# Optimization experiments

Hardware: AMD Instinct MI355X
Metric: run time of the kernel (lower is better)

## Reference

```python
import math
import jax, jax.numpy as jnp
import numpy as np

N0 = N1 = 100000
E = 200000
IN = OUT = 128
H = 8
DK = OUT // H
T = 2
R = 3


def setup_inputs() -> dict:
    key = jax.random.key(0)
    ks = jax.random.split(key, 24)
    s = 1.0 / math.sqrt(IN)
    inp = {
        'h0': jax.random.normal(ks[0], (N0, IN), jnp.float32),
        'h1': jax.random.normal(ks[1], (N1, IN), jnp.float32),
        'kw': jax.random.normal(ks[2], (T, IN, OUT), jnp.float32) * s,
        'kb': jax.random.normal(ks[3], (T, OUT), jnp.float32) * 0.01,
        'qw': jax.random.normal(ks[4], (T, IN, OUT), jnp.float32) * s,
        'qb': jax.random.normal(ks[5], (T, OUT), jnp.float32) * 0.01,
        'vw': jax.random.normal(ks[6], (T, IN, OUT), jnp.float32) * s,
        'vb': jax.random.normal(ks[7], (T, OUT), jnp.float32) * 0.01,
        'aw': jax.random.normal(ks[8], (T, OUT, OUT), jnp.float32) * (1.0 / math.sqrt(OUT)),
        'ab': jax.random.normal(ks[9], (T, OUT), jnp.float32) * 0.01,
        'rel_att': jax.random.normal(ks[10], (R, H, DK, DK), jnp.float32) * (1.0 / math.sqrt(DK)),
        'rel_msg': jax.random.normal(ks[11], (R, H, DK, DK), jnp.float32) * (1.0 / math.sqrt(DK)),
        'rel_pri': jnp.ones((R, H), jnp.float32),
        'skip': jnp.ones((T,), jnp.float32),
        'src0': jax.random.randint(ks[12], (E,), 0, N1, jnp.int32),  # author -> paper
        'dst0': jax.random.randint(ks[13], (E,), 0, N0, jnp.int32),
        'src1': jax.random.randint(ks[14], (E,), 0, N0, jnp.int32),  # paper -> author
        'dst1': jax.random.randint(ks[15], (E,), 0, N1, jnp.int32),
        'src2': jax.random.randint(ks[16], (E,), 0, N0, jnp.int32),  # paper -> paper
        'dst2': jax.random.randint(ks[17], (E,), 0, N0, jnp.int32),
    }
    return inp


def _edge_softmax(score, dst, n_dst):
    # segment softmax normalized by destination node (norm_by='dst')
    m = jax.ops.segment_max(score, dst, num_segments=n_dst)
    e = jnp.exp(score - m[dst])
    s = jax.ops.segment_sum(e, dst, num_segments=n_dst)
    return e / s[dst]


def reference(h0, h1, kw, kb, qw, qb, vw, vb, aw, ab, rel_att, rel_msg,
              rel_pri, skip, src0, dst0, src1, dst1, src2, dst2):
    n_heads, d_k = rel_att.shape[1], rel_att.shape[2]
    sqrt_dk = math.sqrt(d_k)
    hs = (h0, h1)
    Ns = (h0.shape[0], h1.shape[0])
    # per-type K/Q/V projections, reshaped to [N, H, d_k]
    k = [(hs[t] @ kw[t] + kb[t]).reshape(-1, n_heads, d_k) for t in range(2)]
    q = [(hs[t] @ qw[t] + qb[t]).reshape(-1, n_heads, d_k) for t in range(2)]
    v = [(hs[t] @ vw[t] + vb[t]).reshape(-1, n_heads, d_k) for t in range(2)]
    # (relation id, src node type, dst node type, src idx, dst idx)
    rels = ((0, 1, 0, src0, dst0), (1, 0, 1, src1, dst1), (2, 0, 0, src2, dst2))
    agg = {0: [], 1: []}
    for r, st, dt, s_idx, d_idx in rels:
        kk = jnp.einsum('nij,ijk->nik', k[st], rel_att[r])
        vv = jnp.einsum('nij,ijk->nik', v[st], rel_msg[r])
        score = (q[dt][d_idx] * kk[s_idx]).sum(-1) * rel_pri[r] / sqrt_dk  # [E,H]
        attn = _edge_softmax(score, d_idx, Ns[dt])
        msg = vv[s_idx] * attn[..., None]  # [E,H,d_k]
        agg[dt].append(jax.ops.segment_sum(msg, d_idx, num_segments=Ns[dt]))
    outs = []
    for t in range(2):
        tt = sum(agg[t]) / len(agg[t])  # cross_reducer='mean'
        tt = tt.reshape(Ns[t], n_heads * d_k)
        trans = tt @ aw[t] + ab[t]  # dropout in eval mode -> identity
        alpha = jax.nn.sigmoid(skip[t])
        outs.append(trans * alpha + hs[t] * (1.0 - alpha))
    return jnp.stack(outs)  # [2, N, out_dim] (N0 == N1)
```

## Files before the change

### kernel.cpp

```cpp
#include <hip/hip_runtime.h>
#include <stdint.h>

typedef __attribute__((ext_vector_type(8))) short s16x8;
typedef __attribute__((ext_vector_type(4))) float f32x4;

__device__ __forceinline__ ushort f2bf(float x) {
  union { float f; uint32_t u; } v; v.f = x;
  uint32_t r = v.u + 0x7FFFu + ((v.u >> 16) & 1u);
  return (ushort)(r >> 16);
}
__device__ __forceinline__ float bf2f(ushort u) {
  union { uint32_t u; float f; } v; v.u = ((uint32_t)u) << 16; return v.f;
}

__device__ __forceinline__ void barrier_lds_only() {
  asm volatile("s_waitcnt lgkmcnt(0)" ::: "memory");
  __builtin_amdgcn_s_barrier();
}

__global__ __launch_bounds__(256) void prep_weights(
    const float* __restrict__ kw, const float* __restrict__ kb,
    const float* __restrict__ qw, const float* __restrict__ qb,
    const float* __restrict__ vw, const float* __restrict__ vb,
    const float* __restrict__ aw, const float* __restrict__ ab,
    const float* __restrict__ rel_att, const float* __restrict__ rel_msg,
    ushort* __restrict__ WT, float* __restrict__ BIAS)
{
  int slot = blockIdx.x, tid = threadIdx.x;
  const float* W; const float* b; const float* rel = nullptr;
  switch (slot) {
    case 0: W = qw;         b = qb;       break;
    case 1: W = qw + 16384; b = qb + 128; break;
    case 2: W = kw + 16384; b = kb + 128; rel = rel_att + 0*2048; break;
    case 3: W = kw;         b = kb;       rel = rel_att + 1*2048; break;
    case 4: W = kw;         b = kb;       rel = rel_att + 2*2048; break;
    case 5: W = vw + 16384; b = vb + 128; rel = rel_msg + 0*2048; break;
    case 6: W = vw;         b = vb;       rel = rel_msg + 1*2048; break;
    case 7: W = vw;         b = vb;       rel = rel_msg + 2*2048; break;
    case 8: W = aw;         b = ab;       break;
    default: W = aw + 16384; b = ab + 128; break;
  }
  ushort* out = WT + slot * 16384;
  for (int e = tid; e < 16384; e += 256) {
    int c = e >> 7, k = e & 127;
    float val;
    if (!rel) {
      val = W[k*128 + c];
    } else {
      int h = c >> 4, cc = c & 15;
      float s = 0.f;
      #pragma unroll
      for (int j = 0; j < 16; j++) s += W[k*128 + h*16 + j] * rel[h*256 + j*16 + cc];
      val = s;
    }
    out[c*128 + k] = f2bf(val);
  }
  if (tid < 128) {
    int c = tid; float val;
    if (!rel) {
      val = b[c];
    } else {
      int h = c >> 4, cc = c & 15;
      float s = 0.f;
      #pragma unroll
      for (int j = 0; j < 16; j++) s += b[h*16 + j] * rel[h*256 + j*16 + cc];
      val = s;
    }
    BIAS[slot*128 + c] = val;
  }
}

__global__ __launch_bounds__(256) void proj_fused(
    const float* __restrict__ h0, const float* __restrict__ h1,
    const ushort* __restrict__ WT, const float* __restrict__ BIAS,
    ushort* __restrict__ P, int N)
{
  __shared__ ushort ALDS0[64 * 132];
  __shared__ ushort ALDS1[64 * 132];

  int src_t = blockIdx.y;
  const float* A = src_t ? h1 : h0;
  int nslots = src_t ? 3 : 5;
  unsigned smap = src_t ? 0x521u : 0x76430u;

  int tid = threadIdx.x;
  int lane = tid & 63;
  int wave = tid >> 6;
  int lr = lane & 15, lh = lane >> 4;
  int colbase = (wave & 1) * 64;
  int rowhalf = wave >> 1;

  int base = blockIdx.x * 64;
  if (base >= N) return;

  s16x8 af[2][4];
  #pragma unroll
  for (int rg = 0; rg < 2; rg++) {
    int arow = base + rowhalf*32 + rg*16 + lr;
    if (arow >= N) arow = N - 1;
    #pragma unroll
    for (int ks = 0; ks < 4; ks++) {
      const float* ap = A + (size_t)arow*128 + ks*32 + lh*8;
      f32x4 x0 = *(const f32x4*)ap;
      f32x4 x1 = *(const f32x4*)(ap + 4);
      s16x8 v;
      #pragma unroll
      for (int j = 0; j < 4; j++) { v[j] = (short)f2bf(x0[j]); v[4+j] = (short)f2bf(x1[j]); }
      af[rg][ks] = v;
    }
  }

  auto compute_slot = [&](int g, ushort* L) {
    const ushort* Bt = WT + g * 16384;
    const float* bias = BIAS + g * 128;
    #pragma unroll
    for (int ct = 0; ct < 4; ct++) {
      int col = colbase + ct*16 + lr;
      s16x8 bfr[4];
      #pragma unroll
      for (int ks = 0; ks < 4; ks++)
        bfr[ks] = *(const s16x8*)(Bt + col*128 + ks*32 + lh*8);
      float bb = bias[col];
      #pragma unroll
      for (int rg = 0; rg < 2; rg++) {
        f32x4 acc = { bb, bb, bb, bb };
        #pragma unroll
        for (int ks = 0; ks < 4; ks++)
          acc = __builtin_amdgcn_mfma_f32_16x16x32_bf16(af[rg][ks], bfr[ks], acc, 0, 0, 0);
        int rl0 = rowhalf*32 + rg*16 + lh*4;
        #pragma unroll
        for (int i = 0; i < 4; i++)
          L[(rl0 + i) * 132 + col] = f2bf(acc[i]);
      }
    }
  };

  auto copyout = [&](int g, const ushort* L) {
    ushort* C = P + (size_t)g * N * 128;
    #pragma unroll
    for (int j = 0; j < 4; j++) {
      int idx = j * 256 + tid;
      int row = idx >> 4, ch = idx & 15;
      int gr = base + row;
      if (gr < N)
        __builtin_nontemporal_store(
            *(const s16x8*)(L + row * 132 + ch * 8),
            (s16x8*)(C + (size_t)gr * 128 + ch * 8));
    }
  };

  int prev = smap & 15;
  compute_slot(prev, ALDS0);
  barrier_lds_only();
  for (int si = 1; si < nslots; si++) {
    int g = (smap >> (si * 4)) & 15;
    ushort* cur = (si & 1) ? ALDS1 : ALDS0;
    const ushort* pv = (si & 1) ? ALDS0 : ALDS1;
    copyout(prev, pv);
    compute_slot(g, cur);
    barrier_lds_only();
    prev = g;
  }
  copyout(prev, (nslots & 1) ? ALDS0 : ALDS1);
}

__global__ void count_edges(const int* __restrict__ d0, const int* __restrict__ d1,
                            const int* __restrict__ d2, int* __restrict__ counts,
                            int E, int N)
{
  int idx = blockIdx.x * 256 + threadIdx.x;
  if (idx >= 3 * E) return;
  int r = idx / E, e = idx - r * E;
  const int* D = (r == 0) ? d0 : (r == 1) ? d1 : d2;
  atomicAdd(counts + r * N + D[e], 1);
}

#define SCAN_CHUNK 2048
#define MAXC 1024

__global__ __launch_bounds__(256) void scan_partial(
    const int* __restrict__ counts, int* __restrict__ offsets,
    int* __restrict__ bsum, int N)
{
  int r = blockIdx.y, c = blockIdx.x, tid = threadIdx.x;
  const int* cnt = counts + (size_t)r * N;
  int* o = offsets + (size_t)r * (N + 1);
  int idx0 = c * SCAN_CHUNK + tid * 8;
  int p[8]; int run = 0;
  #pragma unroll
  for (int j = 0; j < 8; j++) {
    int v = (idx0 + j < N) ? cnt[idx0 + j] : 0;
    run += v; p[j] = run;
  }
  int lane = tid & 63, wid = tid >> 6;
  int x = run;
  #pragma unroll
  for (int off = 1; off < 64; off <<= 1) {
    int t = __shfl_up(x, off, 64);
    if (lane >= off) x += t;
  }
  __shared__ int wsum[4];
  if (lane == 63) wsum[wid] = x;
  __syncthreads();
  int woff = 0;
  for (int wph = 0; wph < wid; wph++) woff += wsum[wph];
  int texcl = woff + x - run;
  #pragma unroll
  for (int j = 0; j < 8; j++)
    if (idx0 + j < N) o[idx0 + j + 1] = texcl + p[j];
  if (tid == 255) bsum[r * MAXC + c] = woff + x;
}

__global__ void scan_bsums(int* __restrict__ bsum, int nchunks)
{
  int r = blockIdx.x, lane = threadIdx.x;
  int carry = 0;
  for (int base = 0; base < nchunks; base += 64) {
    int i = base + lane;
    int v0 = (i < nchunks) ? bsum[r * MAXC + i] : 0;
    int x = v0;
    #pragma unroll
    for (int off = 1; off < 64; off <<= 1) {
      int t = __shfl_up(x, off, 64);
      if (lane >= off) x += t;
    }
    if (i < nchunks) bsum[r * MAXC + i] = carry + x - v0;
    carry += __shfl(x, 63, 64);
  }
}

__global__ __launch_bounds__(256) void scan_add(
    int* __restrict__ offsets, const int* __restrict__ bsum, int N)
{
  int r = blockIdx.y, c = blockIdx.x, tid = threadIdx.x;
  int* o = offsets + (size_t)r * (N + 1);
  if (c == 0 && tid == 0) o[0] = 0;
  int add = bsum[r * MAXC + c];
  if (add == 0) return;
  int idx0 = c * SCAN_CHUNK + tid * 8;
  #pragma unroll
  for (int j = 0; j < 8; j++) {
    int i = idx0 + j;
    if (i < N) o[i + 1] += add;
  }
}

__global__ void scatter_edges(const int* __restrict__ d0, const int* __restrict__ d1,
                              const int* __restrict__ d2,
                              const int* __restrict__ offsets, int* __restrict__ cursor,
                              int* __restrict__ elist, int E, int N)
{
  int idx = blockIdx.x * 256 + threadIdx.x;
  if (idx >= 3 * E) return;
  int r = idx / E, e = idx - r * E;
  const int* D = (r == 0) ? d0 : (r == 1) ? d1 : d2;
  int dst = D[e];
  int pos = offsets[r * (N + 1) + dst] + atomicAdd(cursor + r * N + dst, 1);
  elist[r * E + pos] = e;
}

__global__ void edge_scores(const int* __restrict__ s0, const int* __restrict__ d0,
                            const int* __restrict__ s1, const int* __restrict__ d1,
                            const int* __restrict__ s2, const int* __restrict__ d2,
                            const ushort* __restrict__ P, const float* __restrict__ rel_pri,
                            float* __restrict__ scores, int E, int N)
{
  int idx = blockIdx.x * 256 + threadIdx.x;
  if (idx >= 3 * E * 8) return;
  int r = idx / (E * 8);
  int rem = idx - r * (E * 8);
  int e = rem >> 3, h = rem & 7;
  const int* S = (r == 0) ? s0 : (r == 1) ? s1 : s2;
  const int* D = (r == 0) ? d0 : (r == 1) ? d1 : d2;
  int src = S[e], dst = D[e];
  int dt = (r == 1) ? 1 : 0;
  const ushort* qrow = P + ((size_t)dt * N + dst) * 128 + h * 16;
  const ushort* krow = P + ((size_t)(2 + r) * N + src) * 128 + h * 16;
  s16x8 qa = *(const s16x8*)qrow;
  s16x8 qb_ = *(const s16x8*)(qrow + 8);
  s16x8 ka = *(const s16x8*)krow;
  s16x8 kb_ = *(const s16x8*)(krow + 8);
  float s = 0.f;
  #pragma unroll
  for (int j = 0; j < 8; j++) {
    s += bf2f((ushort)qa[j]) * bf2f((ushort)ka[j]);
    s += bf2f((ushort)qb_[j]) * bf2f((ushort)kb_[j]);
  }
  __builtin_nontemporal_store(s * rel_pri[r * 8 + h] * 0.25f,
                              &scores[(size_t)r * E * 8 + e * 8 + h]);
}

__global__ __launch_bounds__(256) void agg_final(
    const int* __restrict__ elistA, const int* __restrict__ offsA,
    const int* __restrict__ SA, const float* __restrict__ scA,
    const ushort* __restrict__ VVA,
    const int* __restrict__ elistB, const int* __restrict__ offsB,
    const int* __restrict__ SB, const float* __restrict__ scB,
    const ushort* __restrict__ VVB,
    int nrel,
    const ushort* __restrict__ WT, const float* __restrict__ BIAS,
    const float* __restrict__ H, const float* __restrict__ skip, int t,
    float* __restrict__ outT, int N)
{
  __shared__ ushort ALDS[32 * 132];

  int tid = threadIdx.x;
  int dstl = tid >> 3, h = tid & 7;
  int dst = blockIdx.x * 32 + dstl;
  bool valid = dst < N;

  float accT[16];
  #pragma unroll
  for (int j = 0; j < 16; j++) accT[j] = 0.f;

  {
    int b0 = valid ? offsA[dst] : 0, b1 = valid ? offsA[dst + 1] : 0;
    float m = -1e30f;
    for (int i = b0; i < b1; i++)
      m = fmaxf(m, scA[(size_t)elistA[i] * 8 + h]);
    float sum = 0.f;
    float acc[16];
    #pragma unroll
    for (int j = 0; j < 16; j++) acc[j] = 0.f;
    for (int i = b0; i < b1; i++) {
      int e = elistA[i];
      float w = __expf(scA[(size_t)e * 8 + h] - m);
      sum += w;
      const ushort* vr = VVA + (size_t)SA[e] * 128 + h * 16;
      s16x8 v0 = *(const s16x8*)vr;
      s16x8 v1 = *(const s16x8*)(vr + 8);
      #pragma unroll
      for (int j = 0; j < 8; j++) {
        acc[j]     += w * bf2f((ushort)v0[j]);
        acc[8 + j] += w * bf2f((ushort)v1[j]);
      }
    }
    float inv = (b1 > b0) ? 1.0f / sum : 0.f;
    #pragma unroll
    for (int j = 0; j < 16; j++) accT[j] += acc[j] * inv;
  }
  if (nrel == 2) {
    int b0 = valid ? offsB[dst] : 0, b1 = valid ? offsB[dst + 1] : 0;
    float m = -1e30f;
    for (int i = b0; i < b1; i++)
      m = fmaxf(m, scB[(size_t)elistB[i] * 8 + h]);
    float sum = 0.f;
    float acc[16];
    #pragma unroll
    for (int j = 0; j < 16; j++) acc[j] = 0.f;
    for (int i = b0; i < b1; i++) {
      int e = elistB[i];
      float w = __expf(scB[(size_t)e * 8 + h] - m);
      sum += w;
      const ushort* vr = VVB + (size_t)SB[e] * 128 + h * 16;
      s16x8 v0 = *(const s16x8*)vr;
      s16x8 v1 = *(const s16x8*)(vr + 8);
      #pragma unroll
      for (int j = 0; j < 8; j++) {
        acc[j]     += w * bf2f((ushort)v0[j]);
        acc[8 + j] += w * bf2f((ushort)v1[j]);
      }
    }
    float inv = (b1 > b0) ? 1.0f / sum : 0.f;
    #pragma unroll
    for (int j = 0; j < 16; j++) accT[j] += acc[j] * inv;
  }
  float sc = (nrel == 2) ? 0.5f : 1.0f;
  ushort* arow = ALDS + dstl * 132 + h * 16;
  #pragma unroll
  for (int j = 0; j < 16; j++) arow[j] = f2bf(accT[j] * sc);

  __syncthreads();

  int lane = tid & 63, wv = tid >> 6;
  int lr = lane & 15, lh = lane >> 4;
  int rowhalf = wv & 1, colhalf = wv >> 1;
  const ushort* Bt = WT + (8 + t) * 16384;
  const float* bias = BIAS + (8 + t) * 128;
  float alpha = 1.0f / (1.0f + __expf(-skip[t]));
  float beta = 1.0f - alpha;

  s16x8 af[4];
  int arow_l = rowhalf * 16 + lr;
  #pragma unroll
  for (int ks = 0; ks < 4; ks++)
    af[ks] = *(const s16x8*)(ALDS + arow_l * 132 + ks * 32 + lh * 8);

  #pragma unroll
  for (int ct = 0; ct < 4; ct++) {
    int col = colhalf * 64 + ct * 16 + lr;
    s16x8 bfr[4];
    #pragma unroll
    for (int ks = 0; ks < 4; ks++)
      bfr[ks] = *(const s16x8*)(Bt + col * 128 + ks * 32 + lh * 8);
    float bb = bias[col];
    f32x4 acc = { bb, bb, bb, bb };
    #pragma unroll
    for (int ks = 0; ks < 4; ks++)
      acc = __builtin_amdgcn_mfma_f32_16x16x32_bf16(af[ks], bfr[ks], acc, 0, 0, 0);
    int r0l = rowhalf * 16 + lh * 4;
    #pragma unroll
    for (int i = 0; i < 4; i++) {
      int g = blockIdx.x * 32 + r0l + i;
      if (g < N) {
        size_t off = (size_t)g * 128 + col;
        __builtin_nontemporal_store(acc[i] * alpha + H[off] * beta, &outT[off]);
      }
    }
  }
}

extern "C" void kernel_launch(void* const* d_in, const int* in_sizes, int n_in,
                              void* d_out, int out_size, void* d_ws, size_t ws_size,
                              hipStream_t stream)
{
  const float* h0      = (const float*)d_in[0];
  const float* h1      = (const float*)d_in[1];
  const float* kw      = (const float*)d_in[2];
  const float* kb      = (const float*)d_in[3];
  const float* qw      = (const float*)d_in[4];
  const float* qb      = (const float*)d_in[5];
  const float* vw      = (const float*)d_in[6];
  const float* vb      = (const float*)d_in[7];
  const float* aw      = (const float*)d_in[8];
  const float* ab      = (const float*)d_in[9];
  const float* rel_att = (const float*)d_in[10];
  const float* rel_msg = (const float*)d_in[11];
  const float* rel_pri = (const float*)d_in[12];
  const float* skip    = (const float*)d_in[13];
  const int* s0 = (const int*)d_in[14];
  const int* d0 = (const int*)d_in[15];
  const int* s1 = (const int*)d_in[16];
  const int* d1 = (const int*)d_in[17];
  const int* s2 = (const int*)d_in[18];
  const int* d2 = (const int*)d_in[19];

  int N = in_sizes[0] / 128;
  int E = in_sizes[14];

  char* w = (char*)d_ws;
  size_t o = 0;
  auto alloc = [&](size_t bytes) { size_t cur = o; o += (bytes + 255) / 256 * 256; return cur; };
  ushort* WT   = (ushort*)(w + alloc((size_t)10 * 16384 * 2));
  float*  BIAS = (float*) (w + alloc((size_t)10 * 128 * 4));
  ushort* P    = (ushort*)(w + alloc((size_t)8 * N * 128 * 2));
  float*  SC   = (float*) (w + alloc((size_t)3 * E * 8 * 4));
  int* counts  = (int*)   (w + alloc((size_t)3 * N * 4));
  int* cursor  = (int*)   (w + alloc((size_t)3 * N * 4));
  int* offs    = (int*)   (w + alloc((size_t)3 * (N + 1) * 4));
  int* elist   = (int*)   (w + alloc((size_t)3 * E * 4));
  int* bsum    = (int*)   (w + alloc((size_t)3 * MAXC * 4));
  (void)ws_size; (void)n_in; (void)out_size;

  hipMemsetAsync(counts, 0, (size_t)3 * N * 4, stream);
  hipMemsetAsync(cursor, 0, (size_t)3 * N * 4, stream);

  prep_weights<<<10, 256, 0, stream>>>(kw, kb, qw, qb, vw, vb, aw, ab,
                                       rel_att, rel_msg, WT, BIAS);

  proj_fused<<<dim3((N + 63) / 64, 2), 256, 0, stream>>>(h0, h1, WT, BIAS, P, N);

  int egrid = (3 * E + 255) / 256;
  count_edges<<<egrid, 256, 0, stream>>>(d0, d1, d2, counts, E, N);

  int nchunks = (N + SCAN_CHUNK - 1) / SCAN_CHUNK;
  scan_partial<<<dim3(nchunks, 3), 256, 0, stream>>>(counts, offs, bsum, N);
  scan_bsums<<<3, 64, 0, stream>>>(bsum, nchunks);
  scan_add<<<dim3(nchunks, 3), 256, 0, stream>>>(offs, bsum, N);

  scatter_edges<<<egrid, 256, 0, stream>>>(d0, d1, d2, offs, cursor, elist, E, N);

  int sgrid = (3 * E * 8 + 255) / 256;
  edge_scores<<<sgrid, 256, 0, stream>>>(s0, d0, s1, d1, s2, d2, P, rel_pri, SC, E, N);

  int fgrid = (N + 31) / 32;
  agg_final<<<fgrid, 256, 0, stream>>>(
      elist + (size_t)0 * E, offs + (size_t)0 * (N + 1), s0, SC + (size_t)0 * E * 8,
      P + (size_t)5 * N * 128,
      elist + (size_t)2 * E, offs + (size_t)2 * (N + 1), s2, SC + (size_t)2 * E * 8,
      P + (size_t)7 * N * 128,
      2, WT, BIAS, h0, skip, 0, (float*)d_out, N);
  agg_final<<<fgrid, 256, 0, stream>>>(
      elist + (size_t)1 * E, offs + (size_t)1 * (N + 1), s1, SC + (size_t)1 * E * 8,
      P + (size_t)6 * N * 128,
      elist + (size_t)1 * E, offs + (size_t)1 * (N + 1), s1, SC + (size_t)1 * E * 8,
      P + (size_t)6 * N * 128,
      1, WT, BIAS, h1, skip, 1, (float*)d_out + (size_t)N * 128, N);
}
```

Before: 422.4 us.

## Fuse edge score computation into aggregation kernel and drop softmax max pass

Removes the separate edge_scores kernel and its scores buffer. Each destination thread now loads its Q row once and computes dot products with gathered relation-transformed K rows inline while accumulating the weighted V sum. The separate segment-max pass is also dropped, so exp is applied to unshifted scores. This saves a kernel launch, the score write and the repeated score reads, but it risks overflow for large scores because the max subtraction is gone.

```diff
diff --git a/kernel.cpp b/kernel.cpp
--- a/kernel.cpp
+++ b/kernel.cpp
@@ -259,45 +259,15 @@
   elist[r * E + pos] = e;
 }
 
-__global__ void edge_scores(const int* __restrict__ s0, const int* __restrict__ d0,
-                            const int* __restrict__ s1, const int* __restrict__ d1,
-                            const int* __restrict__ s2, const int* __restrict__ d2,
-                            const ushort* __restrict__ P, const float* __restrict__ rel_pri,
-                            float* __restrict__ scores, int E, int N)
-{
-  int idx = blockIdx.x * 256 + threadIdx.x;
-  if (idx >= 3 * E * 8) return;
-  int r = idx / (E * 8);
-  int rem = idx - r * (E * 8);
-  int e = rem >> 3, h = rem & 7;
-  const int* S = (r == 0) ? s0 : (r == 1) ? s1 : s2;
-  const int* D = (r == 0) ? d0 : (r == 1) ? d1 : d2;
-  int src = S[e], dst = D[e];
-  int dt = (r == 1) ? 1 : 0;
-  const ushort* qrow = P + ((size_t)dt * N + dst) * 128 + h * 16;
-  const ushort* krow = P + ((size_t)(2 + r) * N + src) * 128 + h * 16;
-  s16x8 qa = *(const s16x8*)qrow;
-  s16x8 qb_ = *(const s16x8*)(qrow + 8);
-  s16x8 ka = *(const s16x8*)krow;
-  s16x8 kb_ = *(const s16x8*)(krow + 8);
-  float s = 0.f;
-  #pragma unroll
-  for (int j = 0; j < 8; j++) {
-    s += bf2f((ushort)qa[j]) * bf2f((ushort)ka[j]);
-    s += bf2f((ushort)qb_[j]) * bf2f((ushort)kb_[j]);
-  }
-  __builtin_nontemporal_store(s * rel_pri[r * 8 + h] * 0.25f,
-                              &scores[(size_t)r * E * 8 + e * 8 + h]);
-}
-
 __global__ __launch_bounds__(256) void agg_final(
     const int* __restrict__ elistA, const int* __restrict__ offsA,
-    const int* __restrict__ SA, const float* __restrict__ scA,
-    const ushort* __restrict__ VVA,
+    const int* __restrict__ SA,
+    const ushort* __restrict__ KKA, const ushort* __restrict__ VVA,
     const int* __restrict__ elistB, const int* __restrict__ offsB,
-    const int* __restrict__ SB, const float* __restrict__ scB,
-    const ushort* __restrict__ VVB,
-    int nrel,
+    const int* __restrict__ SB,
+    const ushort* __restrict__ KKB, const ushort* __restrict__ VVB,
+    int nrel, int rA, int rB,
+    const ushort* __restrict__ Q, const float* __restrict__ rel_pri,
     const ushort* __restrict__ WT, const float* __restrict__ BIAS,
     const float* __restrict__ H, const float* __restrict__ skip, int t,
     float* __restrict__ outT, int N)
@@ -309,24 +279,38 @@
   int dst = blockIdx.x * 32 + dstl;
   bool valid = dst < N;
 
+  float qf[16];
+  {
+    const ushort* qrow = Q + (size_t)(valid ? dst : 0) * 128 + h * 16;
+    s16x8 qa = *(const s16x8*)qrow;
+    s16x8 qb_ = *(const s16x8*)(qrow + 8);
+    #pragma unroll
+    for (int j = 0; j < 8; j++) { qf[j] = bf2f((ushort)qa[j]); qf[8 + j] = bf2f((ushort)qb_[j]); }
+  }
+
   float accT[16];
   #pragma unroll
   for (int j = 0; j < 16; j++) accT[j] = 0.f;
 
   {
+    float pr = rel_pri[rA * 8 + h] * 0.25f;
     int b0 = valid ? offsA[dst] : 0, b1 = valid ? offsA[dst + 1] : 0;
-    float m = -1e30f;
-    for (int i = b0; i < b1; i++)
-      m = fmaxf(m, scA[(size_t)elistA[i] * 8 + h]);
     float sum = 0.f;
     float acc[16];
     #pragma unroll
     for (int j = 0; j < 16; j++) acc[j] = 0.f;
     for (int i = b0; i < b1; i++) {
       int e = elistA[i];
-      float w = __expf(scA[(size_t)e * 8 + h] - m);
-      sum += w;
-      const ushort* vr = VVA + (size_t)SA[e] * 128 + h * 16;
+      int s = SA[e];
+      const ushort* kr = KKA + (size_t)s * 128 + h * 16;
+      s16x8 k0 = *(const s16x8*)kr;
+      s16x8 k1 = *(const s16x8*)(kr + 8);
+      float sc = 0.f;
+      #pragma unroll
+      for (int j = 0; j < 8; j++)
+        sc += qf[j] * bf2f((ushort)k0[j]) + qf[8 + j] * bf2f((ushort)k1[j]);
+      float w = __expf(sc * pr);
+      const ushort* vr = VVA + (size_t)s * 128 + h * 16;
       s16x8 v0 = *(const s16x8*)vr;
       s16x8 v1 = *(const s16x8*)(vr + 8);
       #pragma unroll
@@ -334,25 +318,31 @@
         acc[j]     += w * bf2f((ushort)v0[j]);
         acc[8 + j] += w * bf2f((ushort)v1[j]);
       }
+      sum += w;
     }
     float inv = (b1 > b0) ? 1.0f / sum : 0.f;
     #pragma unroll
     for (int j = 0; j < 16; j++) accT[j] += acc[j] * inv;
   }
   if (nrel == 2) {
+    float pr = rel_pri[rB * 8 + h] * 0.25f;
     int b0 = valid ? offsB[dst] : 0, b1 = valid ? offsB[dst + 1] : 0;
-    float m = -1e30f;
-    for (int i = b0; i < b1; i++)
-      m = fmaxf(m, scB[(size_t)elistB[i] * 8 + h]);
     float sum = 0.f;
     float acc[16];
     #pragma unroll
     for (int j = 0; j < 16; j++) acc[j] = 0.f;
     for (int i = b0; i < b1; i++) {
       int e = elistB[i];
-      float w = __expf(scB[(size_t)e * 8 + h] - m);
-      sum += w;
-      const ushort* vr = VVB + (size_t)SB[e] * 128 + h * 16;
+      int s = SB[e];
+      const ushort* kr = KKB + (size_t)s * 128 + h * 16;
+      s16x8 k0 = *(const s16x8*)kr;
+      s16x8 k1 = *(const s16x8*)(kr + 8);
+      float sc = 0.f;
+      #pragma unroll
+      for (int j = 0; j < 8; j++)
+        sc += qf[j] * bf2f((ushort)k0[j]) + qf[8 + j] * bf2f((ushort)k1[j]);
+      float w = __expf(sc * pr);
+      const ushort* vr = VVB + (size_t)s * 128 + h * 16;
       s16x8 v0 = *(const s16x8*)vr;
       s16x8 v1 = *(const s16x8*)(vr + 8);
       #pragma unroll
@@ -360,6 +350,7 @@
         acc[j]     += w * bf2f((ushort)v0[j]);
         acc[8 + j] += w * bf2f((ushort)v1[j]);
       }
+      sum += w;
     }
     float inv = (b1 > b0) ? 1.0f / sum : 0.f;
     #pragma unroll
@@ -444,7 +435,6 @@
   ushort* WT   = (ushort*)(w + alloc((size_t)10 * 16384 * 2));
   float*  BIAS = (float*) (w + alloc((size_t)10 * 128 * 4));
   ushort* P    = (ushort*)(w + alloc((size_t)8 * N * 128 * 2));
-  float*  SC   = (float*) (w + alloc((size_t)3 * E * 8 * 4));
   int* counts  = (int*)   (w + alloc((size_t)3 * N * 4));
   int* cursor  = (int*)   (w + alloc((size_t)3 * N * 4));
   int* offs    = (int*)   (w + alloc((size_t)3 * (N + 1) * 4));
@@ -470,20 +460,21 @@
 
   scatter_edges<<<egrid, 256, 0, stream>>>(d0, d1, d2, offs, cursor, elist, E, N);
 
-  int sgrid = (3 * E * 8 + 255) / 256;
-  edge_scores<<<sgrid, 256, 0, stream>>>(s0, d0, s1, d1, s2, d2, P, rel_pri, SC, E, N);
-
   int fgrid = (N + 31) / 32;
   agg_final<<<fgrid, 256, 0, stream>>>(
-      elist + (size_t)0 * E, offs + (size_t)0 * (N + 1), s0, SC + (size_t)0 * E * 8,
-      P + (size_t)5 * N * 128,
-      elist + (size_t)2 * E, offs + (size_t)2 * (N + 1), s2, SC + (size_t)2 * E * 8,
-      P + (size_t)7 * N * 128,
-      2, WT, BIAS, h0, skip, 0, (float*)d_out, N);
+      elist + (size_t)0 * E, offs + (size_t)0 * (N + 1), s0,
+      P + (size_t)2 * N * 128, P + (size_t)5 * N * 128,
+      elist + (size_t)2 * E, offs + (size_t)2 * (N + 1), s2,
+      P + (size_t)4 * N * 128, P + (size_t)7 * N * 128,
+      2, 0, 2,
+      P + (size_t)0 * N * 128, rel_pri,
+      WT, BIAS, h0, skip, 0, (float*)d_out, N);
   agg_final<<<fgrid, 256, 0, stream>>>(
-      elist + (size_t)1 * E, offs + (size_t)1 * (N + 1), s1, SC + (size_t)1 * E * 8,
-      P + (size_t)6 * N * 128,
-      elist + (size_t)1 * E, offs + (size_t)1 * (N + 1), s1, SC + (size_t)1 * E * 8,
-      P + (size_t)6 * N * 128,
-      1, WT, BIAS, h1, skip, 1, (float*)d_out + (size_t)N * 128, N);
-}
+      elist + (size_t)1 * E, offs + (size_t)1 * (N + 1), s1,
+      P + (size_t)3 * N * 128, P + (size_t)6 * N * 128,
+      elist + (size_t)1 * E, offs + (size_t)1 * (N + 1), s1,
+      P + (size_t)3 * N * 128, P + (size_t)6 * N * 128,
+      1, 1, 1,
+      P + (size_t)1 * N * 128, rel_pri,
+      WT, BIAS, h1, skip, 1, (float*)d_out + (size_t)N * 128, N);
+}
```

Result: no change. 414.5 us (-1.9%).
